# Performance work log

Measured on AMD Instinct MI355X. Metric: run time of the kernel, lower is better.

The kernel has to match this reference:

```python
import jax, jax.numpy as jnp
import numpy as np

N = 50000      # num nodes
E = 400000     # directed edges (avg out-degree 8)
DIN = 128
DOUT = 128
ALPHA = 0.5    # args.alphaDir (buffer, requires_grad=False)
BETA = 0.5     # args.betaDir
GAMA = 0.5     # args.gamaDir


def _dedupe(rows, cols, vals, n):
    key = rows.astype(np.int64) * n + cols.astype(np.int64)
    uk, inv = np.unique(key, return_inverse=True)
    v = np.bincount(inv, weights=vals, minlength=uk.shape[0])
    return (uk // n).astype(np.int32), (uk % n).astype(np.int32), v.astype(np.float32)


def _dir_norm(r, c, v, n):
    # directed_norm: D_out^{-1/2} A D_in^{-1/2}, inf -> 0
    in_deg = np.bincount(c, weights=v, minlength=n)
    out_deg = np.bincount(r, weights=v, minlength=n)
    in_is = np.zeros(n); m = in_deg > 0; in_is[m] = in_deg[m] ** -0.5
    out_is = np.zeros(n); m = out_deg > 0; out_is[m] = out_deg[m] ** -0.5
    return r, c, (out_is[r] * v * in_is[c]).astype(np.float32)


def _spgemm(rA, cA, vA, rB, cB, vB, n):
    # sparse @ sparse in COO, vectorized numpy
    order = np.argsort(rB, kind='stable')
    rBs, cBs, vBs = rB[order], cB[order], vB[order]
    degB = np.bincount(rBs, minlength=n)
    indptr = np.concatenate(([0], np.cumsum(degB)))
    counts = degB[cA]
    total = int(counts.sum())
    rep = np.repeat(np.arange(len(rA)), counts)
    first = np.cumsum(counts) - counts
    pos = np.arange(total) - np.repeat(first, counts) + np.repeat(indptr[cA], counts)
    rows = rA[rep]
    cols = cBs[pos]
    vals = vA[rep].astype(np.float64) * vBs[pos]
    return _dedupe(rows, cols, vals, n)


def setup_inputs() -> dict:
    rng = np.random.default_rng(0)
    r0 = rng.integers(0, N, E).astype(np.int64)
    c0 = rng.integers(0, N, E).astype(np.int64)
    r, c, v = _dedupe(r0, c0, np.ones(E, np.float32), N)
    a = _dir_norm(r, c, v, N)                 # adj_norm
    at = _dir_norm(c, r, v, N)                # adj_t_norm
    rr, cc, vv = _spgemm(a[0], a[1], a[2], at[0], at[1], at[2], N)
    aat = _dir_norm(rr, cc, vv, N)            # directed_norm(A @ At)
    rr, cc, vv = _spgemm(at[0], at[1], at[2], a[0], a[1], a[2], N)
    ata = _dir_norm(rr, cc, vv, N)            # directed_norm(At @ A)
    rr, cc, vv = _spgemm(a[0], a[1], a[2], a[0], a[1], a[2], N)
    aa = _dir_norm(rr, cc, vv, N)             # directed_norm(A @ A)
    rr, cc, vv = _spgemm(at[0], at[1], at[2], at[0], at[1], at[2], N)
    atat = _dir_norm(rr, cc, vv, N)           # directed_norm(At @ At)

    key = jax.random.key(0)
    ks = jax.random.split(key, 7)
    x = jax.random.normal(ks[0], (N, DIN), dtype=jnp.float32)
    s = 1.0 / np.sqrt(DIN)

    def lin(k):
        k1, k2 = jax.random.split(k)
        w = jax.random.uniform(k1, (DIN, DOUT), jnp.float32, -s, s)
        b = jax.random.uniform(k2, (DOUT,), jnp.float32, -s, s)
        return w, b

    w_sd, b_sd = lin(ks[1]); w_ds, b_ds = lin(ks[2])
    w0, b0 = lin(ks[3]); w1, b1 = lin(ks[4])
    w2, b2 = lin(ks[5]); w3, b3 = lin(ks[6])

    out = {'x': x,
           'w_sd': w_sd, 'b_sd': b_sd, 'w_ds': w_ds, 'b_ds': b_ds,
           'w0': w0, 'b0': b0, 'w1': w1, 'b1': b1,
           'w2': w2, 'b2': b2, 'w3': w3, 'b3': b3}
    for name, t in (('a', a), ('at', at), ('aat', aat), ('ata', ata), ('aa', aa), ('atat', atat)):
        out[name + '_rows'] = jnp.asarray(t[0])
        out[name + '_cols'] = jnp.asarray(t[1])
        out[name + '_vals'] = jnp.asarray(t[2])
    return out


def _spmm(rows, cols, vals, x):
    # (A @ x)[i] = sum_e vals[e] * x[cols[e]] scattered to rows[e]
    return jax.ops.segment_sum(vals[:, None] * x[cols], rows, num_segments=x.shape[0])


def reference(x, a_rows, a_cols, a_vals, at_rows, at_cols, at_vals,
              aat_rows, aat_cols, aat_vals, ata_rows, ata_cols, ata_vals,
              aa_rows, aa_cols, aa_vals, atat_rows, atat_cols, atat_vals,
              w_sd, b_sd, w_ds, b_ds, w0, b0, w1, b1, w2, b2, w3, b3):
    out1 = ALPHA * (_spmm(a_rows, a_cols, a_vals, x) @ w_sd + b_sd) \
         + (1.0 - ALPHA) * (_spmm(at_rows, at_cols, at_vals, x) @ w_ds + b_ds)
    out2 = BETA * (_spmm(aat_rows, aat_cols, aat_vals, x) @ w0 + b0) \
         + (1.0 - BETA) * (_spmm(ata_rows, ata_cols, ata_vals, x) @ w1 + b1)
    out3 = GAMA * (_spmm(aa_rows, aa_cols, aa_vals, x) @ w2 + b2) \
         + (1.0 - GAMA) * (_spmm(atat_rows, atat_cols, atat_vals, x) @ w3 + b3)
    return out1 + out2 + out3
```

## Files before the change

### kernel.cpp

```cpp
#include <hip/hip_runtime.h>
#include <hip/hip_bf16.h>

#define FD 128

typedef __attribute__((ext_vector_type(8))) short bf16x8;
typedef __attribute__((ext_vector_type(4))) float f32x4;

__device__ __forceinline__ float bfu2f(unsigned short u) {
  return __uint_as_float(((unsigned int)u) << 16);
}
__device__ __forceinline__ float b2f(__hip_bfloat16 v) { return __bfloat162float(v); }
__device__ __forceinline__ unsigned int pk2(float lo, float hi) {
  return (unsigned int)__bfloat16_as_ushort(__float2bfloat16(lo)) |
         ((unsigned int)__bfloat16_as_ushort(__float2bfloat16(hi)) << 16);
}

__device__ __forceinline__ float ldf(const void* p, int i, int ff) {
  return ff ? ((const float*)p)[i] : b2f(((const __hip_bfloat16*)p)[i]);
}
__device__ __forceinline__ int ldi(const void* p, int i, int fi) {
  return fi ? (int)((const long long*)p)[i] : ((const int*)p)[i];
}

__global__ void cvtall_k(const void* __restrict__ rows, const void* __restrict__ cols,
                         const void* __restrict__ vals, int nnz, int n,
                         const void* __restrict__ x,
                         int* __restrict__ r32, int* __restrict__ c32,
                         float* __restrict__ vf, int* __restrict__ cntT,
                         int* flags) {
  __shared__ int cnt[2];
  if (threadIdx.x < 2) cnt[threadIdx.x] = 0;
  __syncthreads();
  const unsigned short* xu = (const unsigned short*)x;
  int big = 0;
  for (int i = threadIdx.x; i < 1024; i += 256) {
    int e = (xu[i] >> 7) & 0xFF;
    if (e >= 0x90) big++;
  }
  if (big) atomicAdd(&cnt[0], big);
  const int* ci = (const int*)cols;
  int zeros = 0;
  for (int i = threadIdx.x; i < 128; i += 256)
    if ((i & 1) && ci[i] == 0) zeros++;
  if (zeros) atomicAdd(&cnt[1], zeros);
  __syncthreads();
  int ff = (cnt[0] > 16) ? 1 : 0;
  int fi = (cnt[1] >= 32) ? 1 : 0;
  if (blockIdx.x == 0 && threadIdx.x == 0) {
    flags[0] = ff;
    flags[1] = fi;
  }
  int i = blockIdx.x * 256 + threadIdx.x;
  if (i >= nnz) return;
  int r = ldi(rows, i, fi);
  int c = ldi(cols, i, fi);
  if ((unsigned)r >= (unsigned)n) r = 0;
  if ((unsigned)c >= (unsigned)n) c = 0;
  r32[i] = r;
  c32[i] = c;
  vf[i] = ldf(vals, i, ff);
  atomicAdd(&cntT[c], 1);
}

__global__ void scanAbs_k(const int* __restrict__ cnt, int n, int* bsum,
                          const int* __restrict__ rows, int nnz, int* rpA, int nb) {
  int blk = blockIdx.x;
  if (blk < nb) {
    __shared__ int sh[256];
    int t = threadIdx.x;
    int i = blk * 256 + t;
    sh[t] = (i < n) ? cnt[i] : 0;
    __syncthreads();
    for (int d = 128; d > 0; d >>= 1) {
      if (t < d) sh[t] += sh[t + d];
      __syncthreads();
    }
    if (t == 0) bsum[blk] = sh[0];
  } else {
    int i = (blk - nb) * 256 + threadIdx.x;
    if (i > n) return;
    int lo = 0, hi = nnz;
    while (lo < hi) { int mid = (lo + hi) >> 1; if (rows[mid] < i) lo = mid + 1; else hi = mid; }
    rpA[i] = lo;
  }
}

__global__ void scanB_k(int* bsum, int nb, int* rpTail) {
  __shared__ int sh[256];
  int t = threadIdx.x;
  int v = (t < nb) ? bsum[t] : 0;
  sh[t] = v;
  __syncthreads();
  int val = v;
  for (int d = 1; d < 256; d <<= 1) {
    int add = (t >= d) ? sh[t - d] : 0;
    __syncthreads();
    val += add;
    sh[t] = val;
    __syncthreads();
  }
  if (t < nb) bsum[t] = val - v;
  if (t == 255) *rpTail = val;
}

__global__ void scanC_k(const int* __restrict__ cnt, int n, const int* __restrict__ bsum,
                        int* rp, int* cur) {
  __shared__ int sh[256];
  int t = threadIdx.x;
  int i = blockIdx.x * 256 + t;
  int v = (i < n) ? cnt[i] : 0;
  sh[t] = v;
  __syncthreads();
  int val = v;
  for (int d = 1; d < 256; d <<= 1) {
    int add = (t >= d) ? sh[t - d] : 0;
    __syncthreads();
    val += add;
    sh[t] = val;
    __syncthreads();
  }
  int ex = val - v + bsum[blockIdx.x];
  if (i < n) { rp[i] = ex; cur[i] = ex; }
}

__global__ void scatter_k(const int* __restrict__ r, const int* __restrict__ c,
                          const float* __restrict__ v, int nnz,
                          int* cur, int* tSrc, float* tVal) {
  int i = blockIdx.x * 256 + threadIdx.x;
  if (i >= nnz) return;
  int p = atomicAdd(&cur[c[i]], 1);
  if ((unsigned)p >= (unsigned)nnz) return;
  tSrc[p] = r[i];
  tVal[p] = v[i];
}

__global__ void nodesum_k(const int* __restrict__ rpA, const float* __restrict__ av,
                          const int* __restrict__ rpT, const float* __restrict__ tv,
                          float* __restrict__ u1, float* __restrict__ v1, int n) {
  int i = blockIdx.x * 256 + threadIdx.x;
  if (i >= n) return;
  float su = 0.f;
  int e0 = rpA[i], e1 = rpA[i + 1];
  for (int j = e0; j < e1; ++j) su += av[j];
  u1[i] = su;
  float sv = 0.f;
  int f0 = rpT[i], f1 = rpT[i + 1];
  for (int j = f0; j < f1; ++j) sv += tv[j];
  v1[i] = sv;
}

__global__ void bias_k(const void* a, const void* b, const void* c, const void* d,
                       const void* e, const void* f, float* bias, const int* flags) {
  int ff = flags[0];
  int i = threadIdx.x;
  bias[i] = 0.5f * (ldf(a, i, ff) + ldf(b, i, ff) + ldf(c, i, ff)
                  + ldf(d, i, ff) + ldf(e, i, ff) + ldf(f, i, ff));
}

__global__ void fill_k(unsigned short* o, int n) {
  int i = blockIdx.x * 256 + threadIdx.x;
  if (i < n) o[i] = 0x3E80;
}

struct W6p { const void* w[6]; };
struct B6p { const void* b[6]; };

__global__ void dpp_k(const int* __restrict__ rpA, const int* __restrict__ ci,
                      const float* __restrict__ av,
                      const int* __restrict__ rpT, const int* __restrict__ ti,
                      const float* __restrict__ tv,
                      const float* __restrict__ u1, const float* __restrict__ v1,
                      float* __restrict__ s1, float* __restrict__ s2,
                      float* __restrict__ s3, float* __restrict__ s4, int n,
                      const void* __restrict__ x, unsigned int* __restrict__ xb, int nx,
                      W6p ws, __hip_bfloat16* __restrict__ Wt,
                      B6p bs, float* __restrict__ bias,
                      const int* flags, int nb, int cvtB) {
  int blk = blockIdx.x;
  if (blk < nb) {
    int i = blk * 256 + threadIdx.x;
    if (i >= n) return;
    float a1 = 0.f, a3 = 0.f;
    int s0 = rpA[i], se = rpA[i + 1];
    for (int j = s0; j < se; ++j) {
      int c = ci[j];
      float v = av[j];
      a1 = fmaf(v, v1[c], a1);
      a3 = fmaf(v, u1[c], a3);
    }
    s1[i] = (a1 > 0.f) ? rsqrtf(a1) : 0.f;
    s3[i] = (a3 > 0.f) ? rsqrtf(a3) : 0.f;
    float a2 = 0.f, a4 = 0.f;
    int t0 = rpT[i], t1 = rpT[i + 1];
    for (int j = t0; j < t1; ++j) {
      int r = ti[j];
      float v = tv[j];
      a2 = fmaf(v, u1[r], a2);
      a4 = fmaf(v, v1[r], a4);
    }
    s2[i] = (a2 > 0.f) ? rsqrtf(a2) : 0.f;
    s4[i] = (a4 > 0.f) ? rsqrtf(a4) : 0.f;
    return;
  }
  int ff = flags[0];
  if (blk < nb + cvtB) {
    int i = ((blk - nb) * 256 + threadIdx.x) * 8;
    if (i >= nx) return;
    uint4 o;
    if (ff) {
      float4 p0 = *(const float4*)((const float*)x + i);
      float4 p1 = *(const float4*)((const float*)x + i + 4);
      o.x = pk2(p0.x, p0.y); o.y = pk2(p0.z, p0.w);
      o.z = pk2(p1.x, p1.y); o.w = pk2(p1.z, p1.w);
    } else {
      o = *(const uint4*)((const unsigned short*)x + i);
    }
    *(uint4*)(xb + i / 2) = o;
    return;
  }
  if (blk < nb + cvtB + 384) {
    int e = (blk - nb - cvtB) * 256 + threadIdx.x;
    if (e >= 6 * 16384) return;
    int seg = e >> 14;
    int r = e & 16383;
    int nn = r >> 7;
    int innerB = (r & 127) << 1;
    int kb = innerB ^ ((nn & 7) << 4);
    int k = kb >> 1;
    Wt[e] = __float2bfloat16(ldf(ws.w[seg], k * 128 + nn, ff));
    return;
  }
  int i = threadIdx.x;
  if (i < FD)
    bias[i] = 0.5f * (ldf(bs.b[0], i, ff) + ldf(bs.b[1], i, ff) + ldf(bs.b[2], i, ff)
                    + ldf(bs.b[3], i, ff) + ldf(bs.b[4], i, ff) + ldf(bs.b[5], i, ff));
}

struct FHSet {
  const int* rp; const int* ci; const float* cv;
  unsigned int* ot; unsigned int* oa; unsigned int* ob;
  const float* sA; const float* sB;
};

__global__ __launch_bounds__(256) void fh3d_k(
    FHSet h0, FHSet h1, const unsigned int* __restrict__ xb, int n, int half) {
  int blk = blockIdx.x;
  bool hiH = blk >= half;
  const int* rp = hiH ? h1.rp : h0.rp;
  const int* ci = hiH ? h1.ci : h0.ci;
  const float* cv = hiH ? h1.cv : h0.cv;
  unsigned int* ot = hiH ? h1.ot : h0.ot;
  unsigned int* oa = hiH ? h1.oa : h0.oa;
  unsigned int* ob = hiH ? h1.ob : h0.ob;
  const float* sA = hiH ? h1.sA : h0.sA;
  const float* sB = hiH ? h1.sB : h0.sB;
  int bb = hiH ? blk - half : blk;

  int wave = threadIdx.x >> 6;
  int l = threadIdx.x & 63;
  int lf = l & 31;
  bool hlo = l < 32;
  int r = bb * 4 + wave;
  if (r >= n) return;
  int s = rp[r], e = rp[r + 1];

  float t0 = 0.f, t1 = 0.f, t2 = 0.f, t3 = 0.f;
  float a0 = 0.f, a1 = 0.f, a2 = 0.f, a3 = 0.f;
  float b0 = 0.f, b1 = 0.f, b2 = 0.f, b3 = 0.f;

  int j = s;
  for (; j + 1 < e; j += 2) {
    int cA = ci[j], cB = ci[j + 1];
    float vA = cv[j], vB = cv[j + 1];
    int c = hlo ? cA : cB;
    float v = hlo ? vA : vB;
    float va = v * sA[c];
    float vb = v * sB[c];
    uint2 xu = *(const uint2*)(xb + (size_t)c * 64 + lf * 2);
    float f0 = __uint_as_float(xu.x << 16);
    float f1 = __uint_as_float(xu.x & 0xFFFF0000u);
    float f2 = __uint_as_float(xu.y << 16);
    float f3 = __uint_as_float(xu.y & 0xFFFF0000u);
    t0 = fmaf(v, f0, t0); t1 = fmaf(v, f1, t1); t2 = fmaf(v, f2, t2); t3 = fmaf(v, f3, t3);
    a0 = fmaf(va, f0, a0); a1 = fmaf(va, f1, a1); a2 = fmaf(va, f2, a2); a3 = fmaf(va, f3, a3);
    b0 = fmaf(vb, f0, b0); b1 = fmaf(vb, f1, b1); b2 = fmaf(vb, f2, b2); b3 = fmaf(vb, f3, b3);
  }
  if (j < e && hlo) {
    int c = ci[j];
    float v = cv[j];
    float va = v * sA[c];
    float vb = v * sB[c];
    uint2 xu = *(const uint2*)(xb + (size_t)c * 64 + lf * 2);
    float f0 = __uint_as_float(xu.x << 16);
    float f1 = __uint_as_float(xu.x & 0xFFFF0000u);
    float f2 = __uint_as_float(xu.y << 16);
    float f3 = __uint_as_float(xu.y & 0xFFFF0000u);
    t0 = fmaf(v, f0, t0); t1 = fmaf(v, f1, t1); t2 = fmaf(v, f2, t2); t3 = fmaf(v, f3, t3);
    a0 = fmaf(va, f0, a0); a1 = fmaf(va, f1, a1); a2 = fmaf(va, f2, a2); a3 = fmaf(va, f3, a3);
    b0 = fmaf(vb, f0, b0); b1 = fmaf(vb, f1, b1); b2 = fmaf(vb, f2, b2); b3 = fmaf(vb, f3, b3);
  }
  t0 += __shfl_xor(t0, 32); t1 += __shfl_xor(t1, 32);
  t2 += __shfl_xor(t2, 32); t3 += __shfl_xor(t3, 32);
  a0 += __shfl_xor(a0, 32); a1 += __shfl_xor(a1, 32);
  a2 += __shfl_xor(a2, 32); a3 += __shfl_xor(a3, 32);
  b0 += __shfl_xor(b0, 32); b1 += __shfl_xor(b1, 32);
  b2 += __shfl_xor(b2, 32); b3 += __shfl_xor(b3, 32);

  if (hlo) {
    uint2 o;
    o.x = pk2(t0, t1); o.y = pk2(t2, t3);
    *(uint2*)(ot + (size_t)r * 64 + lf * 2) = o;
    o.x = pk2(a0, a1); o.y = pk2(a2, a3);
    *(uint2*)(oa + (size_t)r * 128 + lf * 2) = o;
  } else {
    uint2 o;
    o.x = pk2(b0, b1); o.y = pk2(b2, b3);
    *(uint2*)(ob + (size_t)r * 128 + lf * 2) = o;
  }
}

struct SHSet {
  const int* rp; const int* ci; const float* cv;
  const unsigned int* gp;
  unsigned int* ya; unsigned int* yb;
  const float* rsa; const float* rsb;
};

__global__ __launch_bounds__(256) void sh2d_k(SHSet h0, SHSet h1, int n, int half) {
  int blk = blockIdx.x;
  bool hiH = blk >= half;
  const int* rp = hiH ? h1.rp : h0.rp;
  const int* ci = hiH ? h1.ci : h0.ci;
  const float* cv = hiH ? h1.cv : h0.cv;
  const unsigned int* gp = hiH ? h1.gp : h0.gp;
  unsigned int* ya = hiH ? h1.ya : h0.ya;
  unsigned int* yb = hiH ? h1.yb : h0.yb;
  const float* rsa = hiH ? h1.rsa : h0.rsa;
  const float* rsb = hiH ? h1.rsb : h0.rsb;
  int bb = hiH ? blk - half : blk;

  int wave = threadIdx.x >> 6;
  int l = threadIdx.x & 63;
  int lf = l & 31;
  bool hlo = l < 32;
  int r = bb * 4 + wave;
  if (r >= n) return;
  int s = rp[r], e = rp[r + 1];

  float f0 = 0.f, f1 = 0.f, f2 = 0.f, f3 = 0.f;
  int j = s;
  for (; j + 3 < e; j += 4) {
#pragma unroll
    for (int u = 0; u < 4; ++u) {
      int c = ci[j + u];
      float v = cv[j + u];
      uint2 g = *(const uint2*)(gp + (size_t)c * 128 + l * 2);
      f0 = fmaf(v, __uint_as_float(g.x << 16), f0);
      f1 = fmaf(v, __uint_as_float(g.x & 0xFFFF0000u), f1);
      f2 = fmaf(v, __uint_as_float(g.y << 16), f2);
      f3 = fmaf(v, __uint_as_float(g.y & 0xFFFF0000u), f3);
    }
  }
  for (; j < e; ++j) {
    int c = ci[j];
    float v = cv[j];
    uint2 g = *(const uint2*)(gp + (size_t)c * 128 + l * 2);
    f0 = fmaf(v, __uint_as_float(g.x << 16), f0);
    f1 = fmaf(v, __uint_as_float(g.x & 0xFFFF0000u), f1);
    f2 = fmaf(v, __uint_as_float(g.y << 16), f2);
    f3 = fmaf(v, __uint_as_float(g.y & 0xFFFF0000u), f3);
  }
  float rs = hlo ? rsa[r] : rsb[r];
  unsigned int* yp = hlo ? ya : yb;
  uint2 o;
  o.x = pk2(f0 * rs, f1 * rs);
  o.y = pk2(f2 * rs, f3 * rs);
  *(uint2*)(yp + (size_t)r * 64 + lf * 2) = o;
}

struct Y6 { const unsigned short* y[6]; };

__global__ __launch_bounds__(256) void gemm6m3_k(
    Y6 ys, const unsigned short* __restrict__ Wt2, const float* __restrict__ bias,
    void* __restrict__ outp, int M, const int* flags) {
  int ff = flags[0];
  __shared__ __align__(16) unsigned short Bs[16384];
  const int tid = threadIdx.x;
  const int lane = tid & 63;
  const int wave = tid >> 6;
  const int m = lane & 15;
  const int q = lane >> 4;
  const int r0 = blockIdx.x * 128 + wave * 32;
  const int row0 = r0 + m;
  const int row1 = r0 + 16 + m;
  const bool ok0 = row0 < M;
  const bool ok1 = row1 < M;
  const bf16x8 zero8 = {0, 0, 0, 0, 0, 0, 0, 0};

  f32x4 acc0[8], acc1[8];
#pragma unroll
  for (int nt = 0; nt < 8; ++nt) {
    acc0[nt] = (f32x4){0.f, 0.f, 0.f, 0.f};
    acc1[nt] = (f32x4){0.f, 0.f, 0.f, 0.f};
  }

  bf16x8 Bst[8];
#pragma unroll
  for (int c2 = 0; c2 < 8; ++c2)
    Bst[c2] = *(const bf16x8*)(Wt2 + (size_t)(c2 * 256 + tid) * 8);
  bf16x8 Ap0[4], Ap1[4];
#pragma unroll
  for (int kc = 0; kc < 4; ++kc) {
    Ap0[kc] = ok0 ? *(const bf16x8*)(ys.y[0] + (size_t)row0 * FD + kc * 32 + q * 8) : zero8;
    Ap1[kc] = ok1 ? *(const bf16x8*)(ys.y[0] + (size_t)row1 * FD + kc * 32 + q * 8) : zero8;
  }

  const int swz = (m & 7) << 4;

#pragma unroll
  for (int t = 0; t < 6; ++t) {
    __syncthreads();
#pragma unroll
    for (int c2 = 0; c2 < 8; ++c2)
      *(bf16x8*)((char*)Bs + (size_t)(c2 * 256 + tid) * 16) = Bst[c2];
    bf16x8 A0[4], A1[4];
#pragma unroll
    for (int kc = 0; kc < 4; ++kc) { A0[kc] = Ap0[kc]; A1[kc] = Ap1[kc]; }
    if (t < 5) {
#pragma unroll
      for (int c2 = 0; c2 < 8; ++c2)
        Bst[c2] = *(const bf16x8*)(Wt2 + (size_t)(t + 1) * 16384 +
                                   (size_t)(c2 * 256 + tid) * 8);
#pragma unroll
      for (int kc = 0; kc < 4; ++kc) {
        Ap0[kc] = ok0 ? *(const bf16x8*)(ys.y[t + 1] + (size_t)row0 * FD + kc * 32 + q * 8) : zero8;
        Ap1[kc] = ok1 ? *(const bf16x8*)(ys.y[t + 1] + (size_t)row1 * FD + kc * 32 + q * 8) : zero8;
      }
    }
    __syncthreads();
#pragma unroll
    for (int kc = 0; kc < 4; ++kc) {
      const int koff = (kc * 64 + q * 16) ^ swz;
#pragma unroll
      for (int nt = 0; nt < 8; ++nt) {
        const int nrow = nt * 16 + m;
        bf16x8 bfv = *(const bf16x8*)((const char*)Bs + nrow * 256 + koff);
        acc0[nt] = __builtin_amdgcn_mfma_f32_16x16x32_bf16(A0[kc], bfv, acc0[nt], 0, 0, 0);
        acc1[nt] = __builtin_amdgcn_mfma_f32_16x16x32_bf16(A1[kc], bfv, acc1[nt], 0, 0, 0);
      }
    }
  }

#pragma unroll
  for (int nt = 0; nt < 8; ++nt) {
    int col = nt * 16 + m;
    float bv = bias[col];
#pragma unroll
    for (int rg = 0; rg < 4; ++rg) {
      int g0 = r0 + q * 4 + rg;
      if (g0 < M) {
        float v = 0.5f * acc0[nt][rg] + bv;
        if (ff) ((float*)outp)[(size_t)g0 * FD + col] = v;
        else ((unsigned short*)outp)[(size_t)g0 * FD + col] =
            __bfloat16_as_ushort(__float2bfloat16(v));
      }
      int g1 = r0 + 16 + q * 4 + rg;
      if (g1 < M) {
        float v = 0.5f * acc1[nt][rg] + bv;
        if (ff) ((float*)outp)[(size_t)g1 * FD + col] = v;
        else ((unsigned short*)outp)[(size_t)g1 * FD + col] =
            __bfloat16_as_ushort(__float2bfloat16(v));
      }
    }
  }
}

__global__ __launch_bounds__(128) void spmm_k(
    const int* __restrict__ rp, const void* __restrict__ ci, int cif,
    const void* __restrict__ cv, int cvf,
    const void* __restrict__ x, int xf, __hip_bfloat16* __restrict__ y,
    int n, int nnzMax,
    const float* __restrict__ cscale, const float* __restrict__ rscale,
    const int* flags) {
  int ff = flags[0], fi = flags[1];
  int vf = cvf ? 1 : ff;
  int iw = cif ? fi : 0;
  int xw = xf ? ff : 0;
  const int t = threadIdx.x;
  int r0 = blockIdx.x * 4;
  int rend = min(r0 + 4, n);
  for (int r = r0; r < rend; ++r) {
    int s = rp[r], e = rp[r + 1];
    s = max(0, min(s, nnzMax));
    e = max(s, min(e, nnzMax));
    float acc = 0.f;
    for (int j = s; j < e; ++j) {
      int c = ldi(ci, j, iw);
      if ((unsigned)c >= (unsigned)n) c = 0;
      float v = (vf ? ((const float*)cv)[j] : b2f(((const __hip_bfloat16*)cv)[j]));
      if (cscale) v *= cscale[c];
      float xv = xw ? ((const float*)x)[c * FD + t]
                    : b2f(((const __hip_bfloat16*)x)[c * FD + t]);
      acc = fmaf(v, xv, acc);
    }
    if (rscale) acc *= rscale[r];
    y[r * FD + t] = __float2bfloat16(acc);
  }
}

__global__ __launch_bounds__(256) void gemm_k(
    const __hip_bfloat16* __restrict__ Y, const void* __restrict__ W,
    const float* __restrict__ bias, const void* __restrict__ accin,
    void* __restrict__ outp, int M, const int* flags) {
  int ff = flags[0];
  __shared__ __align__(16) float Wl[32 * 128];
  __shared__ __align__(16) float Yl[64 * 36];
  const int t = threadIdx.x;
  const int row0 = blockIdx.x * 64;
  const int c4 = (t & 31) * 4;
  const int r8 = (t >> 5) * 8;
  const int rs = t >> 3;
  const int q = t & 7;
  float acc[8][4];
#pragma unroll
  for (int m = 0; m < 8; ++m)
#pragma unroll
    for (int j = 0; j < 4; ++j) acc[m][j] = 0.f;
  for (int kc = 0; kc < 4; ++kc) {
    if (ff) {
      const float4* Wg4 = (const float4*)((const float*)W + kc * 32 * 128);
#pragma unroll
      for (int i = 0; i < 4; ++i)
        *(float4*)(Wl + (t + i * 256) * 4) = Wg4[t + i * 256];
    } else {
      const ushort4* Wg4 = (const ushort4*)((const unsigned short*)W + kc * 32 * 128);
#pragma unroll
      for (int i = 0; i < 4; ++i) {
        ushort4 u = Wg4[t + i * 256];
        int base = (t + i * 256) * 4;
        Wl[base + 0] = bfu2f(u.x);
        Wl[base + 1] = bfu2f(u.y);
        Wl[base + 2] = bfu2f(u.z);
        Wl[base + 3] = bfu2f(u.w);
      }
    }
#pragma unroll
    for (int i = 0; i < 2; ++i) {
      int rr = rs + i * 32;
      int grow = row0 + rr;
      ushort4 u = make_ushort4(0, 0, 0, 0);
      if (grow < M)
        u = *(const ushort4*)((const unsigned short*)Y + grow * FD + kc * 32 + q * 4);
      float* yd = Yl + rr * 36 + q * 4;
      yd[0] = bfu2f(u.x); yd[1] = bfu2f(u.y); yd[2] = bfu2f(u.z); yd[3] = bfu2f(u.w);
    }
    __syncthreads();
#pragma unroll
    for (int kk = 0; kk < 32; kk += 4) {
      float4 w0 = *(const float4*)(Wl + (kk + 0) * 128 + c4);
      float4 w1 = *(const float4*)(Wl + (kk + 1) * 128 + c4);
      float4 w2 = *(const float4*)(Wl + (kk + 2) * 128 + c4);
      float4 w3 = *(const float4*)(Wl + (kk + 3) * 128 + c4);
#pragma unroll
      for (int m = 0; m < 8; ++m) {
        float4 yv = *(const float4*)(Yl + (r8 + m) * 36 + kk);
        acc[m][0] = fmaf(yv.x, w0.x, acc[m][0]);
        acc[m][1] = fmaf(yv.x, w0.y, acc[m][1]);
        acc[m][2] = fmaf(yv.x, w0.z, acc[m][2]);
        acc[m][3] = fmaf(yv.x, w0.w, acc[m][3]);
        acc[m][0] = fmaf(yv.y, w1.x, acc[m][0]);
        acc[m][1] = fmaf(yv.y, w1.y, acc[m][1]);
        acc[m][2] = fmaf(yv.y, w1.z, acc[m][2]);
        acc[m][3] = fmaf(yv.y, w1.w, acc[m][3]);
        acc[m][0] = fmaf(yv.z, w2.x, acc[m][0]);
        acc[m][1] = fmaf(yv.z, w2.y, acc[m][1]);
        acc[m][2] = fmaf(yv.z, w2.z, acc[m][2]);
        acc[m][3] = fmaf(yv.z, w2.w, acc[m][3]);
        acc[m][0] = fmaf(yv.w, w3.x, acc[m][0]);
        acc[m][1] = fmaf(yv.w, w3.y, acc[m][1]);
        acc[m][2] = fmaf(yv.w, w3.z, acc[m][2]);
        acc[m][3] = fmaf(yv.w, w3.w, acc[m][3]);
      }
    }
    __syncthreads();
  }
  float4 b4 = make_float4(0.f, 0.f, 0.f, 0.f);
  if (bias) b4 = *(const float4*)(bias + c4);
#pragma unroll
  for (int m = 0; m < 8; ++m) {
    int grow = row0 + r8 + m;
    if (grow >= M) continue;
    float4 rv;
    rv.x = 0.5f * acc[m][0] + b4.x;
    rv.y = 0.5f * acc[m][1] + b4.y;
    rv.z = 0.5f * acc[m][2] + b4.z;
    rv.w = 0.5f * acc[m][3] + b4.w;
    if (accin) {
      if (ff) {
        float4 o = *(const float4*)((const float*)accin + grow * FD + c4);
        rv.x += o.x; rv.y += o.y; rv.z += o.z; rv.w += o.w;
      } else {
        ushort4 o = *(const ushort4*)((const unsigned short*)accin + grow * FD + c4);
        rv.x += bfu2f(o.x); rv.y += bfu2f(o.y); rv.z += bfu2f(o.z); rv.w += bfu2f(o.w);
      }
    }
    if (ff) {
      *(float4*)((float*)outp + grow * FD + c4) = rv;
    } else {
      ushort4 so;
      so.x = __bfloat16_as_ushort(__float2bfloat16(rv.x));
      so.y = __bfloat16_as_ushort(__float2bfloat16(rv.y));
      so.z = __bfloat16_as_ushort(__float2bfloat16(rv.z));
      so.w = __bfloat16_as_ushort(__float2bfloat16(rv.w));
      *(ushort4*)((unsigned short*)outp + grow * FD + c4) = so;
    }
  }
}

extern "C" void kernel_launch(void* const* d_in, const int* in_sizes, int n_in,
                              void* d_out, int out_size, void* d_ws, size_t ws_size,
                              hipStream_t stream) {
  const void* x    = d_in[0];
  const void* w_sd = d_in[1];
  const void* b_sd = d_in[2];
  const void* w_ds = d_in[3];
  const void* b_ds = d_in[4];
  const void* w0   = d_in[5];
  const void* b0   = d_in[6];
  const void* w1   = d_in[7];
  const void* b1   = d_in[8];
  const void* w2   = d_in[9];
  const void* b2   = d_in[10];
  const void* w3   = d_in[11];
  const void* b3   = d_in[12];
  const void* a_rows = d_in[13];
  const void* a_cols = d_in[14];
  const void* a_vals = d_in[15];
  const int nnz = in_sizes[13];
  const int N = in_sizes[0] / FD;

  const size_t BUF = ((size_t)N * FD * 2 + 255) & ~(size_t)255;

  auto misc_need = [&](int nbig) -> size_t {
    size_t need = (size_t)nbig * BUF;
    need += ((size_t)10 * N * 4 + 255) & ~(size_t)255;
    need += 512 + 256 + 1024;
    need += (((size_t)(N + 1) * 4 + 255) & ~(size_t)255) * 2;
    need += (((size_t)N * 4 + 255) & ~(size_t)255) * 2;
    need += (((size_t)nnz * 4 + 255) & ~(size_t)255) * 5;
    need += (6 * 16384 * 2 + 255) & ~(size_t)255;
    return need;
  };
  size_t needA = misc_need(10);
  size_t needB = misc_need(2);

  int pathA = (ws_size >= needA) ? 1 : 0;
  if (!pathA && ws_size < needB) {
    fill_k<<<(out_size + 255) / 256, 256, 0, stream>>>((unsigned short*)d_out, out_size);
    return;
  }

  int nbig = pathA ? 10 : 2;
  char* p = (char*)d_ws;
  char* bufs[10];
  for (int i = 0; i < 10; ++i) bufs[i] = (i < nbig) ? (p + (size_t)i * BUF) : nullptr;
  char* q = p + (size_t)nbig * BUF;
  auto take = [&](size_t bytes) -> char* {
    char* r = q;
    q += (bytes + 255) & ~(size_t)255;
    return r;
  };
  float* degf  = (float*)take((size_t)10 * N * 4);
  float* biasf = (float*)take(512);
  int*   flags = (int*)take(256);
  int*   bsum  = (int*)take(1024);
  int* rpA  = (int*)take((size_t)(N + 1) * 4);
  int* rpT  = (int*)take((size_t)(N + 1) * 4);
  int* curT = (int*)take((size_t)N * 4);
  int* cntT = (int*)take((size_t)N * 4);
  int* tSrc = (int*)take((size_t)nnz * 4);
  float* tValF = (float*)take((size_t)nnz * 4);
  int* aRow32 = (int*)take((size_t)nnz * 4);
  int* aCol32 = (int*)take((size_t)nnz * 4);
  float* aValF = (float*)take((size_t)nnz * 4);
  __hip_bfloat16* Wt = (__hip_bfloat16*)take(6 * 16384 * 2);

  float* u1 = degf;
  float* v1 = degf + N;
  float* s1 = degf + 6 * N;
  float* s2 = degf + 7 * N;
  float* s3 = degf + 8 * N;
  float* s4 = degf + 9 * N;

  int eb = (nnz + 255) / 256;
  int nb = (N + 255) / 256;
  int nb2 = (N + 256) / 256;

  hipMemsetAsync(cntT, 0, (size_t)N * 4, stream);
  cvtall_k<<<eb, 256, 0, stream>>>(a_rows, a_cols, a_vals, nnz, N, x,
                                   aRow32, aCol32, aValF, cntT, flags);
  scanAbs_k<<<nb + nb2, 256, 0, stream>>>(cntT, N, bsum, aRow32, nnz, rpA, nb);
  scanB_k<<<1, 256, 0, stream>>>(bsum, nb, rpT + N);
  scanC_k<<<nb, 256, 0, stream>>>(cntT, N, bsum, rpT, curT);
  scatter_k<<<eb, 256, 0, stream>>>(aRow32, aCol32, aValF, nnz, curT, tSrc, tValF);
  nodesum_k<<<nb, 256, 0, stream>>>(rpA, aValF, rpT, tValF, u1, v1, N);

  int sg2 = (N + 3) / 4;
  int gg = (N + 63) / 64;
  int gg4 = (N + 127) / 128;

  W6p wargs;
  wargs.w[0] = w_sd; wargs.w[1] = w_ds; wargs.w[2] = w0;
  wargs.w[3] = w1;   wargs.w[4] = w2;   wargs.w[5] = w3;
  B6p bargs;
  bargs.b[0] = b_sd; bargs.b[1] = b_ds; bargs.b[2] = b0;
  bargs.b[3] = b1;   bargs.b[4] = b2;   bargs.b[5] = b3;

  if (pathA) {
    unsigned int* xbu = (unsigned int*)bufs[0];
    int nx = N * FD;
    int cvtB = (nx / 8 + 255) / 256;
    dpp_k<<<nb + cvtB + 384 + 1, 256, 0, stream>>>(
        rpA, aCol32, aValF, rpT, tSrc, tValF, u1, v1, s1, s2, s3, s4, N,
        x, xbu, nx, wargs, Wt, bargs, biasf, flags, nb, cvtB);

    unsigned int* t2 = (unsigned int*)bufs[1];
    unsigned int* t1 = (unsigned int*)bufs[2];
    unsigned int* P1 = (unsigned int*)bufs[3];
    unsigned int* P2 = (unsigned int*)bufs[5];
    unsigned int* y3 = (unsigned int*)bufs[7];
    unsigned int* y4 = (unsigned int*)bufs[8];
    unsigned int* y6 = (unsigned int*)bufs[9];
    unsigned int* y5 = (unsigned int*)bufs[0];

    FHSet hT = { rpT, tSrc, tValF, t2, P1, P2 + 64, s1, s3 };
    FHSet hA = { rpA, aCol32, aValF, t1, P2, P1 + 64, s2, s4 };
    fh3d_k<<<2 * sg2, 256, 0, stream>>>(hT, hA, xbu, N, sg2);

    SHSet sA = { rpA, aCol32, aValF, P1, y3, y5, s1, s3 };
    SHSet sT = { rpT, tSrc, tValF, P2, y4, y6, s2, s4 };
    sh2d_k<<<2 * sg2, 256, 0, stream>>>(sA, sT, N, sg2);

    Y6 yargs;
    yargs.y[0] = (const unsigned short*)t1;
    yargs.y[1] = (const unsigned short*)t2;
    yargs.y[2] = (const unsigned short*)y3;
    yargs.y[3] = (const unsigned short*)y4;
    yargs.y[4] = (const unsigned short*)y5;
    yargs.y[5] = (const unsigned short*)y6;
    gemm6m3_k<<<gg4, 256, 0, stream>>>(yargs, (const unsigned short*)Wt, biasf, d_out, N, flags);
  } else {
    dpp_k<<<nb, 256, 0, stream>>>(
        rpA, aCol32, aValF, rpT, tSrc, tValF, u1, v1, s1, s2, s3, s4, N,
        x, (unsigned int*)bufs[0], 0, wargs, Wt, bargs, biasf, flags, nb, 0);
    bias_k<<<1, FD, 0, stream>>>(b_sd, b_ds, b0, b1, b2, b3, biasf, flags);
    __hip_bfloat16* Yb = (__hip_bfloat16*)bufs[0];
    __hip_bfloat16* gb = (__hip_bfloat16*)bufs[1];
    spmm_k<<<sg2, 128, 0, stream>>>(rpA, a_cols, 1, a_vals, 0, x, 1, Yb, N, nnz, nullptr, nullptr, flags);
    gemm_k<<<gg, 256, 0, stream>>>(Yb, w_sd, biasf, nullptr, d_out, N, flags);
    spmm_k<<<sg2, 128, 0, stream>>>(rpT, tSrc, 0, tValF, 1, x, 1, Yb, N, nnz, nullptr, nullptr, flags);
    gemm_k<<<gg, 256, 0, stream>>>(Yb, w_ds, nullptr, d_out, d_out, N, flags);
    spmm_k<<<sg2, 128, 0, stream>>>(rpT, tSrc, 0, tValF, 1, x, 1, gb, N, nnz, s1, nullptr, flags);
    spmm_k<<<sg2, 128, 0, stream>>>(rpA, a_cols, 1, a_vals, 0, gb, 0, Yb, N, nnz, nullptr, s1, flags);
    gemm_k<<<gg, 256, 0, stream>>>(Yb, w0, nullptr, d_out, d_out, N, flags);
    spmm_k<<<sg2, 128, 0, stream>>>(rpA, a_cols, 1, a_vals, 0, x, 1, gb, N, nnz, s2, nullptr, flags);
    spmm_k<<<sg2, 128, 0, stream>>>(rpT, tSrc, 0, tValF, 1, gb, 0, Yb, N, nnz, nullptr, s2, flags);
    gemm_k<<<gg, 256, 0, stream>>>(Yb, w1, nullptr, d_out, d_out, N, flags);
    spmm_k<<<sg2, 128, 0, stream>>>(rpA, a_cols, 1, a_vals, 0, x, 1, gb, N, nnz, s4, nullptr, flags);
    spmm_k<<<sg2, 128, 0, stream>>>(rpA, a_cols, 1, a_vals, 0, gb, 0, Yb, N, nnz, nullptr, s3, flags);
    gemm_k<<<gg, 256, 0, stream>>>(Yb, w2, nullptr, d_out, d_out, N, flags);
    spmm_k<<<sg2, 128, 0, stream>>>(rpT, tSrc, 0, tValF, 1, x, 1, gb, N, nnz, s3, nullptr, flags);
    spmm_k<<<sg2, 128, 0, stream>>>(rpT, tSrc, 0, tValF, 1, gb, 0, Yb, N, nnz, nullptr, s4, flags);
    gemm_k<<<gg, 256, 0, stream>>>(Yb, w3, nullptr, d_out, d_out, N, flags);
  }
}
```

Measured before the change: 444.0 us.

## Precompute per-edge scaled weights and use full-wave row gathers in fh3d

Adds a kernel that precomputes, for each edge, a float4 holding the value and its two column-scaled variants, so fh3d no longer gathers sA/sB per edge. fh3d now has all 64 lanes read one packed bf16 pair of the same neighbour row, with a 4-way unrolled edge loop, in place of half-waves splitting alternate edges and reducing by shuffle. This removes the scattered scale loads and the cross-half reduction. In exchange it adds a kernel launch, two nnz*16-byte workspace arrays, and extra write and read traffic for the packed weights.

```diff
diff --git a/kernel.cpp b/kernel.cpp
--- a/kernel.cpp
+++ b/kernel.cpp
@@ -236,10 +236,27 @@
                     + ldf(bs.b[3], i, ff) + ldf(bs.b[4], i, ff) + ldf(bs.b[5], i, ff));
 }
 
+__global__ void epk_k(const int* __restrict__ cA, const float* __restrict__ vA,
+                      const float* __restrict__ sA1, const float* __restrict__ sA2,
+                      const int* __restrict__ cT, const float* __restrict__ vT,
+                      const float* __restrict__ sT1, const float* __restrict__ sT2,
+                      float4* __restrict__ ewA, float4* __restrict__ ewT, int nnz) {
+  int i = blockIdx.x * 256 + threadIdx.x;
+  if (i < nnz) {
+    int c = cA[i];
+    float v = vA[i];
+    ewA[i] = make_float4(v, v * sA1[c], v * sA2[c], 0.f);
+  } else if (i < 2 * nnz) {
+    int k = i - nnz;
+    int c = cT[k];
+    float v = vT[k];
+    ewT[k] = make_float4(v, v * sT1[c], v * sT2[c], 0.f);
+  }
+}
+
 struct FHSet {
-  const int* rp; const int* ci; const float* cv;
+  const int* rp; const int* ci; const float4* ew;
   unsigned int* ot; unsigned int* oa; unsigned int* ob;
-  const float* sA; const float* sB;
 };
 
 __global__ __launch_bounds__(256) void fh3d_k(
@@ -248,75 +265,46 @@
   bool hiH = blk >= half;
   const int* rp = hiH ? h1.rp : h0.rp;
   const int* ci = hiH ? h1.ci : h0.ci;
-  const float* cv = hiH ? h1.cv : h0.cv;
+  const float4* ew = hiH ? h1.ew : h0.ew;
   unsigned int* ot = hiH ? h1.ot : h0.ot;
   unsigned int* oa = hiH ? h1.oa : h0.oa;
   unsigned int* ob = hiH ? h1.ob : h0.ob;
-  const float* sA = hiH ? h1.sA : h0.sA;
-  const float* sB = hiH ? h1.sB : h0.sB;
   int bb = hiH ? blk - half : blk;
 
   int wave = threadIdx.x >> 6;
   int l = threadIdx.x & 63;
-  int lf = l & 31;
-  bool hlo = l < 32;
   int r = bb * 4 + wave;
   if (r >= n) return;
   int s = rp[r], e = rp[r + 1];
 
-  float t0 = 0.f, t1 = 0.f, t2 = 0.f, t3 = 0.f;
-  float a0 = 0.f, a1 = 0.f, a2 = 0.f, a3 = 0.f;
-  float b0 = 0.f, b1 = 0.f, b2 = 0.f, b3 = 0.f;
-
+  float tl = 0.f, th = 0.f, al = 0.f, ah = 0.f, bl = 0.f, bh = 0.f;
   int j = s;
-  for (; j + 1 < e; j += 2) {
-    int cA = ci[j], cB = ci[j + 1];
-    float vA = cv[j], vB = cv[j + 1];
-    int c = hlo ? cA : cB;
-    float v = hlo ? vA : vB;
-    float va = v * sA[c];
-    float vb = v * sB[c];
-    uint2 xu = *(const uint2*)(xb + (size_t)c * 64 + lf * 2);
-    float f0 = __uint_as_float(xu.x << 16);
-    float f1 = __uint_as_float(xu.x & 0xFFFF0000u);
-    float f2 = __uint_as_float(xu.y << 16);
-    float f3 = __uint_as_float(xu.y & 0xFFFF0000u);
-    t0 = fmaf(v, f0, t0); t1 = fmaf(v, f1, t1); t2 = fmaf(v, f2, t2); t3 = fmaf(v, f3, t3);
-    a0 = fmaf(va, f0, a0); a1 = fmaf(va, f1, a1); a2 = fmaf(va, f2, a2); a3 = fmaf(va, f3, a3);
-    b0 = fmaf(vb, f0, b0); b1 = fmaf(vb, f1, b1); b2 = fmaf(vb, f2, b2); b3 = fmaf(vb, f3, b3);
-  }
-  if (j < e && hlo) {
+  for (; j + 3 < e; j += 4) {
+#pragma unroll
+    for (int u = 0; u < 4; ++u) {
+      int c = ci[j + u];
+      float4 w = ew[j + u];
+      unsigned int xu = xb[(size_t)c * 64 + l];
+      float lo = __uint_as_float(xu << 16);
+      float hi = __uint_as_float(xu & 0xFFFF0000u);
+      tl = fmaf(w.x, lo, tl); th = fmaf(w.x, hi, th);
+      al = fmaf(w.y, lo, al); ah = fmaf(w.y, hi, ah);
+      bl = fmaf(w.z, lo, bl); bh = fmaf(w.z, hi, bh);
+    }
+  }
+  for (; j < e; ++j) {
     int c = ci[j];
-    float v = cv[j];
-    float va = v * sA[c];
-    float vb = v * sB[c];
-    uint2 xu = *(const uint2*)(xb + (size_t)c * 64 + lf * 2);
-    float f0 = __uint_as_float(xu.x << 16);
-    float f1 = __uint_as_float(xu.x & 0xFFFF0000u);
-    float f2 = __uint_as_float(xu.y << 16);
-    float f3 = __uint_as_float(xu.y & 0xFFFF0000u);
-    t0 = fmaf(v, f0, t0); t1 = fmaf(v, f1, t1); t2 = fmaf(v, f2, t2); t3 = fmaf(v, f3, t3);
-    a0 = fmaf(va, f0, a0); a1 = fmaf(va, f1, a1); a2 = fmaf(va, f2, a2); a3 = fmaf(va, f3, a3);
-    b0 = fmaf(vb, f0, b0); b1 = fmaf(vb, f1, b1); b2 = fmaf(vb, f2, b2); b3 = fmaf(vb, f3, b3);
-  }
-  t0 += __shfl_xor(t0, 32); t1 += __shfl_xor(t1, 32);
-  t2 += __shfl_xor(t2, 32); t3 += __shfl_xor(t3, 32);
-  a0 += __shfl_xor(a0, 32); a1 += __shfl_xor(a1, 32);
-  a2 += __shfl_xor(a2, 32); a3 += __shfl_xor(a3, 32);
-  b0 += __shfl_xor(b0, 32); b1 += __shfl_xor(b1, 32);
-  b2 += __shfl_xor(b2, 32); b3 += __shfl_xor(b3, 32);
-
-  if (hlo) {
-    uint2 o;
-    o.x = pk2(t0, t1); o.y = pk2(t2, t3);
-    *(uint2*)(ot + (size_t)r * 64 + lf * 2) = o;
-    o.x = pk2(a0, a1); o.y = pk2(a2, a3);
-    *(uint2*)(oa + (size_t)r * 128 + lf * 2) = o;
-  } else {
-    uint2 o;
-    o.x = pk2(b0, b1); o.y = pk2(b2, b3);
-    *(uint2*)(ob + (size_t)r * 128 + lf * 2) = o;
-  }
+    float4 w = ew[j];
+    unsigned int xu = xb[(size_t)c * 64 + l];
+    float lo = __uint_as_float(xu << 16);
+    float hi = __uint_as_float(xu & 0xFFFF0000u);
+    tl = fmaf(w.x, lo, tl); th = fmaf(w.x, hi, th);
+    al = fmaf(w.y, lo, al); ah = fmaf(w.y, hi, ah);
+    bl = fmaf(w.z, lo, bl); bh = fmaf(w.z, hi, bh);
+  }
+  ot[(size_t)r * 64 + l] = pk2(tl, th);
+  oa[(size_t)r * 128 + l] = pk2(al, ah);
+  ob[(size_t)r * 128 + l] = pk2(bl, bh);
 }
 
 struct SHSet {
@@ -649,6 +637,7 @@
     need += (((size_t)N * 4 + 255) & ~(size_t)255) * 2;
     need += (((size_t)nnz * 4 + 255) & ~(size_t)255) * 5;
     need += (6 * 16384 * 2 + 255) & ~(size_t)255;
+    need += (((size_t)nnz * 16 + 255) & ~(size_t)255) * 2;
     return need;
   };
   size_t needA = misc_need(10);
@@ -684,6 +673,8 @@
   int* aCol32 = (int*)take((size_t)nnz * 4);
   float* aValF = (float*)take((size_t)nnz * 4);
   __hip_bfloat16* Wt = (__hip_bfloat16*)take(6 * 16384 * 2);
+  float4* ewA = (float4*)take((size_t)nnz * 16);
+  float4* ewT = (float4*)take((size_t)nnz * 16);
 
   float* u1 = degf;
   float* v1 = degf + N;
@@ -723,6 +714,8 @@
     dpp_k<<<nb + cvtB + 384 + 1, 256, 0, stream>>>(
         rpA, aCol32, aValF, rpT, tSrc, tValF, u1, v1, s1, s2, s3, s4, N,
         x, xbu, nx, wargs, Wt, bargs, biasf, flags, nb, cvtB);
+    epk_k<<<(2 * nnz + 255) / 256, 256, 0, stream>>>(
+        aCol32, aValF, s2, s4, tSrc, tValF, s1, s3, ewA, ewT, nnz);
 
     unsigned int* t2 = (unsigned int*)bufs[1];
     unsigned int* t1 = (unsigned int*)bufs[2];
@@ -733,8 +726,8 @@
     unsigned int* y6 = (unsigned int*)bufs[9];
     unsigned int* y5 = (unsigned int*)bufs[0];
 
-    FHSet hT = { rpT, tSrc, tValF, t2, P1, P2 + 64, s1, s3 };
-    FHSet hA = { rpA, aCol32, aValF, t1, P2, P1 + 64, s2, s4 };
+    FHSet hT = { rpT, tSrc, ewT, t2, P1, P2 + 64 };
+    FHSet hA = { rpA, aCol32, ewA, t1, P2, P1 + 64 };
     fh3d_k<<<2 * sg2, 256, 0, stream>>>(hT, hA, xbu, N, sg2);
 
     SHSet sA = { rpA, aCol32, aValF, P1, y3, y5, s1, s3 };
```

Result: no change. 440.9 us (-0.7%).
